# Kernel tuning notes

Measured on AMD Instinct MI355X. Metric: run time of the kernel, lower is better.

The kernel has to match this reference:

```python
import jax, jax.numpy as jnp
import numpy as np

B, S, D, H = 2, 2048, 1024, 16
DH = D // H  # d_head = 64
EPS = 1e-6


def _rms_norm(x, eps=EPS):
    # norm_without_weight: RMS normalization over last dim, no learned scale
    return x * jax.lax.rsqrt(jnp.mean(x * x, axis=-1, keepdims=True) + eps)


def _rope_tables(seq_len, dim):
    # angular_freq: dim//4 geometric freqs + dim//4 zeros -> dim//2 total
    freqs = (1.0 / 1024.0) ** jnp.linspace(0.0, 1.0, dim // 4, dtype=jnp.float32)
    freqs = jnp.concatenate([freqs, jnp.zeros((dim // 4,), dtype=jnp.float32)])
    theta = jnp.outer(jnp.arange(seq_len, dtype=jnp.float32), freqs)  # [S, dim//2]
    return jnp.cos(theta), jnp.sin(theta)


def _apply_rope(x_bhsk, cos, sin):
    # x: [B,H,S,DH]; cos/sin: [S, DH//2] broadcast over batch/heads
    c = cos[None, None, :, :]
    s = sin[None, None, :, :]
    xf = x_bhsk.astype(jnp.float32)
    x1, x2 = jnp.split(xf, 2, axis=-1)
    y1 = x1 * c + x2 * s
    y2 = -x1 * s + x2 * c
    return jnp.concatenate([y1, y2], axis=-1).astype(x_bhsk.dtype)


def setup_inputs() -> dict:
    key = jax.random.key(0)
    k0, k1, k2, k3, k4 = jax.random.split(key, 5)
    scale = 1.0 / np.sqrt(D)
    x = jax.random.normal(k0, (B, S, D), dtype=jnp.float32)
    # equinox Linear stores weight as [out_features, in_features], y = x @ W.T
    w_q = jax.random.normal(k1, (D, D), dtype=jnp.float32) * scale
    w_k = jax.random.normal(k2, (D, D), dtype=jnp.float32) * scale
    w_v = jax.random.normal(k3, (D, D), dtype=jnp.float32) * scale
    w_o = jax.random.normal(k4, (D, D), dtype=jnp.float32) * scale
    mask = jnp.tril(jnp.ones((S, S), dtype=bool))  # causal
    return {"x": x, "w_q": w_q, "w_k": w_k, "w_v": w_v, "w_o": w_o, "mask": mask}


def reference(x, w_q, w_k, w_v, w_o, mask):
    b, s, d = x.shape
    # projections (no bias); [B,S,D] @ [D,D].T -> [B,S,D] -> [B,H,S,DH]
    def proj(w):
        y = jnp.einsum('bsd,ed->bse', x, w)
        return y.reshape(b, s, H, DH).transpose(0, 2, 1, 3)
    q, k, v = proj(w_q), proj(w_k), proj(w_v)
    # QK-norm (RMS, no weight)
    q = _rms_norm(q)
    k = _rms_norm(k)
    # rotary over sequence axis
    cos, sin = _rope_tables(s, DH)
    q = _apply_rope(q, cos, sin)
    k = _apply_rope(k, cos, sin)
    # scores [B,H,S,S]
    scores = jnp.einsum('bhsk,bhtk->bhst', q, k) / jnp.sqrt(jnp.float32(DH))
    scores = jnp.where(mask[None, None, :, :], scores, -jnp.inf)
    weights = jax.nn.softmax(scores, axis=-1)
    out = jnp.einsum('bhst,bhtk->bhsk', weights, v)  # [B,H,S,DH]
    out = out.transpose(0, 2, 1, 3).reshape(b, s, d)
    return jnp.einsum('bsd,ed->bse', out, w_o)
```

## Files before the change

kernel.cpp:

```cpp
#include <hip/hip_runtime.h>
#include <hip/hip_bf16.h>

#define Bb 2
#define Ss 2048
#define Dd 1024
#define Hh 16
#define Tt ((size_t)Bb*Ss*Dd)
#define WNn ((size_t)Dd*Dd)

typedef short bf16x8 __attribute__((ext_vector_type(8)));
typedef short bf16x4 __attribute__((ext_vector_type(4)));
typedef float floatx4 __attribute__((ext_vector_type(4)));
typedef unsigned short u16;

__device__ inline void gld16(void* lds, const void* g) {
  __builtin_amdgcn_global_load_lds(
      (const __attribute__((address_space(1))) unsigned int*)g,
      (__attribute__((address_space(3))) unsigned int*)lds, 16, 0, 0);
}

__device__ inline float bf2f(u16 u) {
  unsigned int x = ((unsigned int)u) << 16;
  float f; __builtin_memcpy(&f, &x, 4); return f;
}
__device__ inline u16 f2bf(float f) {
  unsigned int x; __builtin_memcpy(&x, &f, 4);
  x = (x + 0x7fff + ((x >> 16) & 1)) >> 16;
  return (u16)x;
}
__device__ inline float u2f(unsigned int x) {
  float f; __builtin_memcpy(&f, &x, 4); return f;
}
__device__ inline unsigned int cvtpk(float lo, float hi) {
  unsigned int r;
  asm("v_cvt_pk_bf16_f32 %0, %1, %2" : "=v"(r) : "v"(lo), "v"(hi));
  return r;
}

__global__ void sniff(const unsigned int* __restrict__ x, unsigned int* __restrict__ flag,
                      int nwords) {
  __shared__ int cnt;
  if (threadIdx.x == 0) cnt = 0;
  __syncthreads();
  int local = 0;
  for (int i = threadIdx.x; i < nwords; i += blockDim.x) {
    unsigned int wd = x[i];
    if (((wd >> 7)  & 0xFFu) == 0xFFu) local++;
    if (((wd >> 23) & 0xFFu) == 0xFFu) local++;
  }
  atomicAdd(&cnt, local);
  __syncthreads();
  if (threadIdx.x == 0) *flag = (cnt >= 64) ? 1u : 0u;
}

__global__ __launch_bounds__(256) void convert_all(
    const void* __restrict__ x,  const void* __restrict__ wq,
    const void* __restrict__ wk, const void* __restrict__ wv,
    const void* __restrict__ wo, u16* __restrict__ dst,
    int smode, const unsigned int* __restrict__ flag,
    float2* __restrict__ tab) {
  const int gb = blockIdx.x;
  if (gb >= 4096) {
    int e = (gb - 4096)*1024 + threadIdx.x*4;
#pragma unroll
    for (int j = 0; j < 4; j++, e++) {
      int s = e >> 4, f = e & 15;
      float freq = exp2f((-10.0f/15.0f) * (float)f);
      float th = (float)s * freq;
      float sn, c;
      sincosf(th, &sn, &c);
      tab[e] = make_float2(c, sn);
    }
    return;
  }
  const void* src; size_t base; int lb;
  if (gb < 2048)      { src = x;  base = 0;            lb = gb;        }
  else if (gb < 2560) { src = wq; base = Tt;           lb = gb - 2048; }
  else if (gb < 3072) { src = wk; base = Tt + WNn;     lb = gb - 2560; }
  else if (gb < 3584) { src = wv; base = Tt + 2*WNn;   lb = gb - 3072; }
  else                { src = wo; base = Tt + 3*WNn;   lb = gb - 3584; }
  const size_t off = (size_t)lb*2048 + threadIdx.x*8;
  const bool f32 = (smode >= 0) ? (smode == 1) : (*flag != 0u);
  bf16x8 v;
  if (f32) {
    const float* s = (const float*)src + off;
#pragma unroll
    for (int j = 0; j < 8; j++) v[j] = (short)f2bf(s[j]);
  } else {
    v = *(const bf16x8*)((const u16*)src + off);
  }
  *(bf16x8*)(dst + base + off) = v;
}

__global__ __launch_bounds__(256) void gemm_bt(
    const u16* __restrict__ A,
    const u16* __restrict__ W0, const u16* __restrict__ W1, const u16* __restrict__ W2,
    void* __restrict__ C0, void* __restrict__ C1, void* __restrict__ C2,
    int M, int N, int K, const float2* __restrict__ tab)
{
  const u16* W; void* C;
  if (blockIdx.z == 0)      { W = W0; C = C0; }
  else if (blockIdx.z == 1) { W = W1; C = C1; }
  else                      { W = W2; C = C2; }

  __shared__ __align__(16) u16 sA[128*32];
  __shared__ __align__(16) u16 sB[128*32];

  const int tid  = threadIdx.x;
  const int lane = tid & 63;
  const int w    = tid >> 6;
  const int wm = w >> 1, wn = w & 1;
  const int col = lane & 15, quad = lane >> 4;
  const int bm = blockIdx.y, bn = blockIdx.x;

  floatx4 acc[4][4] = {};

  const int c0 = tid, c1 = tid + 256;
  const size_t aOff0 = (size_t)(bm*128 + (c0 >> 2))*K + (c0 & 3)*8;
  const size_t aOff1 = (size_t)(bm*128 + (c1 >> 2))*K + (c1 & 3)*8;
  const size_t bOff0 = (size_t)(bn*128 + (c0 >> 2))*K + (c0 & 3)*8;
  const size_t bOff1 = (size_t)(bn*128 + (c1 >> 2))*K + (c1 & 3)*8;

  for (int kk = 0; kk < K; kk += 32) {
    gld16(&sA[c0*8], A + aOff0 + kk);
    gld16(&sA[c1*8], A + aOff1 + kk);
    gld16(&sB[c0*8], W + bOff0 + kk);
    gld16(&sB[c1*8], W + bOff1 + kk);
    __syncthreads();
    bf16x8 af[4], bfr[4];
#pragma unroll
    for (int i = 0; i < 4; i++)
      af[i] = *(const bf16x8*)&sA[(wm*64 + i*16 + col)*32 + quad*8];
#pragma unroll
    for (int j = 0; j < 4; j++)
      bfr[j] = *(const bf16x8*)&sB[(wn*64 + j*16 + col)*32 + quad*8];
#pragma unroll
    for (int i = 0; i < 4; i++)
#pragma unroll
      for (int j = 0; j < 4; j++)
        acc[i][j] = __builtin_amdgcn_mfma_f32_16x16x32_bf16(af[i], bfr[j], acc[i][j], 0, 0, 0);
    __syncthreads();
  }

  if (blockIdx.z == 2) {
    u16* Ct = (u16*)C;
#pragma unroll
    for (int i = 0; i < 4; i++)
#pragma unroll
      for (int j = 0; j < 4; j++) {
        int d = bn*128 + wn*64 + j*16 + col;
        int g = bm*128 + wm*64 + i*16 + quad*4;
        int hh = d >> 6, dl = d & 63;
        int bb = g >> 11, s = g & (Ss - 1);
        bf16x4 pk;
#pragma unroll
        for (int r = 0; r < 4; r++) pk[r] = (short)f2bf(acc[i][j][r]);
        *(bf16x4*)&Ct[((size_t)(bb*Hh + hh)*64 + dl)*Ss + s] = pk;
      }
  } else {
    const float qs = (blockIdx.z == 0) ? 0.125f : 1.0f;
    u16* Co = (u16*)C;
    const size_t cb = (size_t)(bn*128 + wn*64 + col);
#pragma unroll
    for (int i = 0; i < 4; i++)
#pragma unroll
      for (int r = 0; r < 4; r++) {
        float ss = 0.0f;
#pragma unroll
        for (int j = 0; j < 4; j++) ss += acc[i][j][r]*acc[i][j][r];
        ss += __shfl_xor(ss, 1, 64);
        ss += __shfl_xor(ss, 2, 64);
        ss += __shfl_xor(ss, 4, 64);
        ss += __shfl_xor(ss, 8, 64);
        float rn = rsqrtf(ss*(1.0f/64.0f) + 1e-6f) * qs;
        int grow = bm*128 + wm*64 + i*16 + quad*4 + r;
        float2 cs = tab[(grow & (Ss - 1))*16 + col];
        float c = cs.x, sn = cs.y;
        float x0 = acc[i][0][r]*rn, x1 = acc[i][1][r]*rn;
        float x2 = acc[i][2][r]*rn, x3 = acc[i][3][r]*rn;
        size_t rowb = (size_t)grow*N + cb;
        Co[rowb]      = f2bf(x0*c + x2*sn);
        Co[rowb + 16] = f2bf(x1);
        Co[rowb + 32] = f2bf(x2*c - x0*sn);
        Co[rowb + 48] = f2bf(x3);
      }
  }
}

__global__ __launch_bounds__(256) void gemm_o(
    const u16* __restrict__ A, const u16* __restrict__ W, void* __restrict__ C,
    int M, int N, int K, const unsigned int* __restrict__ flag, int outMode)
{
  __shared__ __align__(16) u16 sA[128*32];
  __shared__ __align__(16) u16 sB[64*32];

  const int tid  = threadIdx.x;
  const int lane = tid & 63;
  const int w    = tid >> 6;
  const int wm = w >> 1, wn = w & 1;
  const int col = lane & 15, quad = lane >> 4;
  const int bm = blockIdx.y, bn = blockIdx.x;

  floatx4 acc[4][2] = {};

  const int c0 = tid, c1 = tid + 256;
  const size_t aOff0 = (size_t)(bm*128 + (c0 >> 2))*K + (c0 & 3)*8;
  const size_t aOff1 = (size_t)(bm*128 + (c1 >> 2))*K + (c1 & 3)*8;
  const size_t bOff0 = (size_t)(bn*64  + (c0 >> 2))*K + (c0 & 3)*8;

  for (int kk = 0; kk < K; kk += 32) {
    gld16(&sA[c0*8], A + aOff0 + kk);
    gld16(&sA[c1*8], A + aOff1 + kk);
    gld16(&sB[c0*8], W + bOff0 + kk);
    __syncthreads();
    bf16x8 af[4], bfr[2];
#pragma unroll
    for (int i = 0; i < 4; i++)
      af[i] = *(const bf16x8*)&sA[(wm*64 + i*16 + col)*32 + quad*8];
#pragma unroll
    for (int j = 0; j < 2; j++)
      bfr[j] = *(const bf16x8*)&sB[(wn*32 + j*16 + col)*32 + quad*8];
#pragma unroll
    for (int i = 0; i < 4; i++)
#pragma unroll
      for (int j = 0; j < 2; j++)
        acc[i][j] = __builtin_amdgcn_mfma_f32_16x16x32_bf16(af[i], bfr[j], acc[i][j], 0, 0, 0);
    __syncthreads();
  }

  const bool f32o = (outMode == 1) || (outMode == -1 && *flag != 0u);
#pragma unroll
  for (int i = 0; i < 4; i++)
#pragma unroll
    for (int j = 0; j < 2; j++)
#pragma unroll
      for (int r = 0; r < 4; r++) {
        int grow = bm*128 + wm*64 + i*16 + quad*4 + r;
        int gcol = bn*64 + wn*32 + j*16 + col;
        size_t idx = (size_t)grow*N + gcol;
        float v = acc[i][j][r];
        if (f32o) ((float*)C)[idx] = v;
        else      ((u16*)C)[idx]   = f2bf(v);
      }
}

__global__ __launch_bounds__(256) void attn(
    const u16* __restrict__ Q, const u16* __restrict__ Kv,
    const u16* __restrict__ Vt, u16* __restrict__ O)
{
  __shared__ __align__(16) u16 sK[2][64*72];
  __shared__ __align__(16) u16 sV[2][2][64*32];
  __shared__ __align__(16) u16 sP[4][16*72];
  __shared__ float sAl[4][16];
  __shared__ float sLi[4][16];

  const int tid  = threadIdx.x;
  const int lane = tid & 63;
  const int w    = tid >> 6;
  const int col = lane & 15, quad = lane >> 4;
  const int bh = blockIdx.x;
  const int qt = 31 - (int)blockIdx.y;
  const int b = bh >> 4, h = bh & 15;
  const size_t base  = (size_t)b*Ss*Dd + (size_t)h*64;
  const size_t vbase = (size_t)bh*64*Ss;

  const int krow = tid >> 2;
  const int kch  = (tid & 3) * 2;
  const int vrow = tid >> 2;
  const int vcp  = (tid & 3) ^ (vrow & 3) ^ ((vrow >> 2) & 3);
  const u16* Vh = Vt + vbase + (size_t)vrow*Ss + vcp*8;
  const int xorv = quad ^ (col & 3) ^ ((col >> 2) & 3);
  u16* sPw = &sP[w][0];
  const float L2E = 1.44269504f;

  const int q0 = qt * 64;
  const int nk = qt + 1;
  const int qg = q0 + w*16 + col;

  bf16x8 qf0, qf1;
  {
    const size_t qoff = base + (size_t)(q0 + w*16 + col)*Dd + quad*8;
    qf0 = *(const bf16x8*)(Q + qoff);
    qf1 = *(const bf16x8*)(Q + qoff + 32);
  }
  floatx4 oacc[4] = {};
  float mi = -1e30f, li = 0.0f;

  {
    const u16* kg = Kv + base + (size_t)krow*Dd + kch*8;
    bf16x8 ka = *(const bf16x8*)kg;
    bf16x8 kb = *(const bf16x8*)(kg + 8);
    gld16(&sV[0][0][tid*8], Vh);
    gld16(&sV[0][1][tid*8], Vh + 32);
    *(bf16x8*)&sK[0][krow*72 + kch*8]     = ka;
    *(bf16x8*)&sK[0][krow*72 + kch*8 + 8] = kb;
    __syncthreads();
  }

  for (int kt = 0; kt < nk; kt++) {
    const int t0 = kt*64;
    const int cur = kt & 1, nxt = cur ^ 1;
    const bool more = (kt + 1 < nk);
    bf16x8 ka, kb;
    if (more) {
      const u16* kg = Kv + base + (size_t)(t0 + 64 + krow)*Dd + kch*8;
      ka = *(const bf16x8*)kg;
      kb = *(const bf16x8*)(kg + 8);
      gld16(&sV[nxt][0][tid*8], Vh + t0 + 64);
      gld16(&sV[nxt][1][tid*8], Vh + t0 + 96);
    }

    floatx4 sc[4] = {};
    __builtin_amdgcn_s_setprio(1);
#pragma unroll
    for (int ts = 0; ts < 4; ts++) {
      bf16x8 k0 = *(const bf16x8*)&sK[cur][(ts*16 + col)*72 + quad*8];
      bf16x8 k1 = *(const bf16x8*)&sK[cur][(ts*16 + col)*72 + 32 + quad*8];
      sc[ts] = __builtin_amdgcn_mfma_f32_16x16x32_bf16(k0, qf0, sc[ts], 0,0,0);
      sc[ts] = __builtin_amdgcn_mfma_f32_16x16x32_bf16(k1, qf1, sc[ts], 0,0,0);
    }
    __builtin_amdgcn_s_setprio(0);

    const bool boundary = (t0 + 63 > q0 + w*16);
    if (boundary) {
      const int tb = t0 + quad*4 - qg;
#pragma unroll
      for (int ts = 0; ts < 4; ts++)
#pragma unroll
        for (int r = 0; r < 4; r++)
          if (tb + ts*16 + r > 0) sc[ts][r] = -1e30f;
    }
    float mx = fmaxf(fmaxf(sc[0][0], sc[0][1]), fmaxf(sc[0][2], sc[0][3]));
#pragma unroll
    for (int ts = 1; ts < 4; ts++)
      mx = fmaxf(mx, fmaxf(fmaxf(sc[ts][0], sc[ts][1]),
                           fmaxf(sc[ts][2], sc[ts][3])));
    mx = fmaxf(mx, __shfl_xor(mx, 16, 64));
    mx = fmaxf(mx, __shfl_xor(mx, 32, 64));
    if (!__all(mx - mi <= 8.0f)) {
      float mn = fmaxf(mi, mx);
      float al = exp2f((mi - mn)*L2E);
      mi = mn; li *= al;
      if (quad == 0) sAl[w][col] = al;
      float a0 = sAl[w][quad*4 + 0], a1 = sAl[w][quad*4 + 1];
      float a2 = sAl[w][quad*4 + 2], a3 = sAl[w][quad*4 + 3];
#pragma unroll
      for (int db = 0; db < 4; db++) {
        oacc[db][0] *= a0; oacc[db][1] *= a1;
        oacc[db][2] *= a2; oacc[db][3] *= a3;
      }
    }
    const float nb = -mi*L2E;
#pragma unroll
    for (int ts = 0; ts < 4; ts++) {
      float p0 = exp2f(fmaf(sc[ts][0], L2E, nb));
      float p1 = exp2f(fmaf(sc[ts][1], L2E, nb));
      float p2 = exp2f(fmaf(sc[ts][2], L2E, nb));
      float p3 = exp2f(fmaf(sc[ts][3], L2E, nb));
      unsigned int pk01 = cvtpk(p0, p1);
      unsigned int pk23 = cvtpk(p2, p3);
      *(uint2*)&sPw[col*72 + ts*16 + quad*4] = make_uint2(pk01, pk23);
      li += (u2f(pk01 << 16) + u2f(pk01 & 0xffff0000u))
          + (u2f(pk23 << 16) + u2f(pk23 & 0xffff0000u));
    }
    bf16x8 pa0 = *(const bf16x8*)&sPw[col*72 + quad*8];
    bf16x8 pa1 = *(const bf16x8*)&sPw[col*72 + 32 + quad*8];
    __builtin_amdgcn_s_setprio(1);
#pragma unroll
    for (int db = 0; db < 4; db++) {
      const int vs = (db*16 + col)*32 + xorv*8;
      bf16x8 vb0 = *(const bf16x8*)&sV[cur][0][vs];
      bf16x8 vb1 = *(const bf16x8*)&sV[cur][1][vs];
      oacc[db] = __builtin_amdgcn_mfma_f32_16x16x32_bf16(pa0, vb0, oacc[db], 0,0,0);
      oacc[db] = __builtin_amdgcn_mfma_f32_16x16x32_bf16(pa1, vb1, oacc[db], 0,0,0);
    }
    __builtin_amdgcn_s_setprio(0);

    if (more) {
      *(bf16x8*)&sK[nxt][krow*72 + kch*8]     = ka;
      *(bf16x8*)&sK[nxt][krow*72 + kch*8 + 8] = kb;
    }
    __syncthreads();
  }

  li += __shfl_xor(li, 16, 64);
  li += __shfl_xor(li, 32, 64);
  if (quad == 0) sLi[w][col] = 1.0f / li;
  float i0 = sLi[w][quad*4 + 0], i1 = sLi[w][quad*4 + 1];
  float i2 = sLi[w][quad*4 + 2], i3 = sLi[w][quad*4 + 3];
#pragma unroll
  for (int db = 0; db < 4; db++) {
    const size_t rb = base + (size_t)(q0 + w*16 + quad*4)*Dd + db*16 + col;
    O[rb]        = f2bf(oacc[db][0] * i0);
    O[rb + Dd]   = f2bf(oacc[db][1] * i1);
    O[rb + 2*Dd] = f2bf(oacc[db][2] * i2);
    O[rb + 3*Dd] = f2bf(oacc[db][3] * i3);
  }
}

extern "C" void kernel_launch(void* const* d_in, const int* in_sizes, int n_in,
                              void* d_out, int out_size, void* d_ws, size_t ws_size,
                              hipStream_t stream) {
  const void* x  = d_in[0];
  const void* wq = d_in[1];
  const void* wk = d_in[2];
  const void* wv = d_in[3];
  const void* wo = d_in[4];

  const size_t T  = Tt;
  const size_t WN = WNn;

  char* ws = (char*)d_ws;
  unsigned int* flag = (unsigned int*)ws;
  u16* xb  = (u16*)(ws + 256);
  u16* wqb = xb  + T;
  u16* wkb = wqb + WN;
  u16* wvb = wkb + WN;
  u16* wob = wvb + WN;
  u16* Qb  = wob + WN;
  u16* Kb  = Qb + T;
  u16* Vb  = Kb + T;
  u16* AO  = Vb + T;
  float2* tab = (float2*)(AO + T);

  int smode = -1;
  if (in_sizes && n_in > 0) {
    if (in_sizes[0] == (int)(T*4))      smode = 1;
    else if (in_sizes[0] == (int)(T*2)) smode = 0;
  }
  if (smode < 0)
    sniff<<<1, 1024, 0, stream>>>((const unsigned int*)x, flag, 65536);

  convert_all<<<4128, 256, 0, stream>>>(x, wq, wk, wv, wo, xb, smode, flag, tab);

  gemm_bt<<<dim3(8, 32, 3), 256, 0, stream>>>(xb, wqb, wkb, wvb, Qb, Kb, Vb,
                                              4096, 1024, 1024, tab);
  attn<<<dim3(32, 32), 256, 0, stream>>>(Qb, Kb, Vb, AO);
  gemm_o<<<dim3(16, 32), 256, 0, stream>>>(AO, wob, d_out,
                                           4096, 1024, 1024, flag, smode);
}
```

Baseline: 233.2 us.

## Double GEMM K-tile to 64 with XOR-swizzled LDS layout

Both projection GEMM kernels now stage 64-wide K slices per iteration instead of 32, which halves the number of barrier pairs per tile. The LDS layout uses an XOR swizzle of the 16-byte chunk index by row, so fragment reads avoid bank conflicts. The cost is twice the LDS per block, which may reduce occupancy, and there is still no double buffering.

```diff
diff --git a/kernel.cpp b/kernel.cpp
--- a/kernel.cpp
+++ b/kernel.cpp
@@ -103,8 +103,8 @@
   else if (blockIdx.z == 1) { W = W1; C = C1; }
   else                      { W = W2; C = C2; }
 
-  __shared__ __align__(16) u16 sA[128*32];
-  __shared__ __align__(16) u16 sB[128*32];
+  __shared__ __align__(16) u16 sA[128*64];
+  __shared__ __align__(16) u16 sB[128*64];
 
   const int tid  = threadIdx.x;
   const int lane = tid & 63;
@@ -115,30 +115,34 @@
 
   floatx4 acc[4][4] = {};
 
-  const int c0 = tid, c1 = tid + 256;
-  const size_t aOff0 = (size_t)(bm*128 + (c0 >> 2))*K + (c0 & 3)*8;
-  const size_t aOff1 = (size_t)(bm*128 + (c1 >> 2))*K + (c1 & 3)*8;
-  const size_t bOff0 = (size_t)(bn*128 + (c0 >> 2))*K + (c0 & 3)*8;
-  const size_t bOff1 = (size_t)(bn*128 + (c1 >> 2))*K + (c1 & 3)*8;
-
-  for (int kk = 0; kk < K; kk += 32) {
-    gld16(&sA[c0*8], A + aOff0 + kk);
-    gld16(&sA[c1*8], A + aOff1 + kk);
-    gld16(&sB[c0*8], W + bOff0 + kk);
-    gld16(&sB[c1*8], W + bOff1 + kk);
-    __syncthreads();
-    bf16x8 af[4], bfr[4];
-#pragma unroll
-    for (int i = 0; i < 4; i++)
-      af[i] = *(const bf16x8*)&sA[(wm*64 + i*16 + col)*32 + quad*8];
-#pragma unroll
-    for (int j = 0; j < 4; j++)
-      bfr[j] = *(const bf16x8*)&sB[(wn*64 + j*16 + col)*32 + quad*8];
-#pragma unroll
-    for (int i = 0; i < 4; i++)
+  const int srow = tid >> 3;
+  const int sch  = (tid & 7) ^ (srow & 7);
+  const size_t aO = (size_t)(bm*128 + srow)*K + sch*8;
+  const size_t bO = (size_t)(bn*128 + srow)*K + sch*8;
+  const int e7 = col & 7;
+
+  for (int kk = 0; kk < K; kk += 64) {
+#pragma unroll
+    for (int j = 0; j < 4; j++) {
+      gld16(&sA[j*2048 + tid*8], A + aO + (size_t)j*32*K + kk);
+      gld16(&sB[j*2048 + tid*8], W + bO + (size_t)j*32*K + kk);
+    }
+    __syncthreads();
+#pragma unroll
+    for (int h = 0; h < 2; h++) {
+      bf16x8 af[4], bfr[4];
+#pragma unroll
+      for (int i = 0; i < 4; i++)
+        af[i] = *(const bf16x8*)&sA[(wm*64 + i*16 + col)*64 + (((h*4 + quad)^e7)*8)];
 #pragma unroll
       for (int j = 0; j < 4; j++)
-        acc[i][j] = __builtin_amdgcn_mfma_f32_16x16x32_bf16(af[i], bfr[j], acc[i][j], 0, 0, 0);
+        bfr[j] = *(const bf16x8*)&sB[(wn*64 + j*16 + col)*64 + (((h*4 + quad)^e7)*8)];
+#pragma unroll
+      for (int i = 0; i < 4; i++)
+#pragma unroll
+        for (int j = 0; j < 4; j++)
+          acc[i][j] = __builtin_amdgcn_mfma_f32_16x16x32_bf16(af[i], bfr[j], acc[i][j], 0, 0, 0);
+    }
     __syncthreads();
   }
 
@@ -191,8 +195,8 @@
     const u16* __restrict__ A, const u16* __restrict__ W, void* __restrict__ C,
     int M, int N, int K, const unsigned int* __restrict__ flag, int outMode)
 {
-  __shared__ __align__(16) u16 sA[128*32];
-  __shared__ __align__(16) u16 sB[64*32];
+  __shared__ __align__(16) u16 sA[128*64];
+  __shared__ __align__(16) u16 sB[64*64];
 
   const int tid  = threadIdx.x;
   const int lane = tid & 63;
@@ -203,28 +207,35 @@
 
   floatx4 acc[4][2] = {};
 
-  const int c0 = tid, c1 = tid + 256;
-  const size_t aOff0 = (size_t)(bm*128 + (c0 >> 2))*K + (c0 & 3)*8;
-  const size_t aOff1 = (size_t)(bm*128 + (c1 >> 2))*K + (c1 & 3)*8;
-  const size_t bOff0 = (size_t)(bn*64  + (c0 >> 2))*K + (c0 & 3)*8;
-
-  for (int kk = 0; kk < K; kk += 32) {
-    gld16(&sA[c0*8], A + aOff0 + kk);
-    gld16(&sA[c1*8], A + aOff1 + kk);
-    gld16(&sB[c0*8], W + bOff0 + kk);
-    __syncthreads();
-    bf16x8 af[4], bfr[2];
-#pragma unroll
-    for (int i = 0; i < 4; i++)
-      af[i] = *(const bf16x8*)&sA[(wm*64 + i*16 + col)*32 + quad*8];
+  const int srow = tid >> 3;
+  const int sch  = (tid & 7) ^ (srow & 7);
+  const size_t aO = (size_t)(bm*128 + srow)*K + sch*8;
+  const size_t bO = (size_t)(bn*64  + srow)*K + sch*8;
+  const int e7 = col & 7;
+
+  for (int kk = 0; kk < K; kk += 64) {
+#pragma unroll
+    for (int j = 0; j < 4; j++)
+      gld16(&sA[j*2048 + tid*8], A + aO + (size_t)j*32*K + kk);
 #pragma unroll
     for (int j = 0; j < 2; j++)
-      bfr[j] = *(const bf16x8*)&sB[(wn*32 + j*16 + col)*32 + quad*8];
-#pragma unroll
-    for (int i = 0; i < 4; i++)
+      gld16(&sB[j*2048 + tid*8], W + bO + (size_t)j*32*K + kk);
+    __syncthreads();
+#pragma unroll
+    for (int h = 0; h < 2; h++) {
+      bf16x8 af[4], bfr[2];
+#pragma unroll
+      for (int i = 0; i < 4; i++)
+        af[i] = *(const bf16x8*)&sA[(wm*64 + i*16 + col)*64 + (((h*4 + quad)^e7)*8)];
 #pragma unroll
       for (int j = 0; j < 2; j++)
-        acc[i][j] = __builtin_amdgcn_mfma_f32_16x16x32_bf16(af[i], bfr[j], acc[i][j], 0, 0, 0);
+        bfr[j] = *(const bf16x8*)&sB[(wn*32 + j*16 + col)*64 + (((h*4 + quad)^e7)*8)];
+#pragma unroll
+      for (int i = 0; i < 4; i++)
+#pragma unroll
+        for (int j = 0; j < 2; j++)
+          acc[i][j] = __builtin_amdgcn_mfma_f32_16x16x32_bf16(af[i], bfr[j], acc[i][j], 0, 0, 0);
+    }
     __syncthreads();
   }
 
```

New measurement: 244.4 us. +4.8%, slower.
